# Performance work log

Measured on AMD Instinct MI355X. Metric: run time of the kernel, lower is better.

Reference implementation:

```python
import jax, jax.numpy as jnp
import numpy as np

N, E = 50000, 800000
IN_C, OUT_C, D_EMB = 64, 64, 64
NEG_SLOPE = 0.2  # GDN GraphLayer default leaky_relu slope


def setup_inputs() -> dict:
    key = jax.random.key(0)
    ks = jax.random.split(key, 9)
    return {
        "x": jax.random.normal(ks[0], (N, IN_C), jnp.float32),
        "edge_index": jax.random.randint(ks[1], (2, E), 0, N, dtype=jnp.int32),
        "embedding": jax.random.normal(ks[2], (N, D_EMB), jnp.float32),
        # learned params of GraphLayer (heads=1, concat)
        "W": jax.random.normal(ks[3], (OUT_C, IN_C), jnp.float32) * (1.0 / np.sqrt(IN_C)),
        "att_i": jax.random.normal(ks[4], (OUT_C,), jnp.float32) * 0.1,
        "att_j": jax.random.normal(ks[5], (OUT_C,), jnp.float32) * 0.1,
        "att_em_i": jax.random.normal(ks[6], (D_EMB,), jnp.float32) * 0.1,
        "att_em_j": jax.random.normal(ks[7], (D_EMB,), jnp.float32) * 0.1,
        "bias": jax.random.normal(ks[8], (OUT_C,), jnp.float32) * 0.01,
    }


def reference(x, edge_index, embedding, W, att_i, att_j, att_em_i, att_em_j, bias):
    n = x.shape[0]
    loops = jnp.arange(n, dtype=edge_index.dtype)
    src = jnp.concatenate([edge_index[0], loops])  # message source j
    dst = jnp.concatenate([edge_index[1], loops])  # message target i

    h = x @ W.T  # [N, OUT_C]
    # per-node attention scores (equivalent to cat(h, emb) . cat(att, att_em))
    s_i = h @ att_i + embedding @ att_em_i  # [N]
    s_j = h @ att_j + embedding @ att_em_j  # [N]

    alpha = s_i[dst] + s_j[src]                         # [E+N] edge logits
    alpha = jax.nn.leaky_relu(alpha, NEG_SLOPE)
    # softmax over incoming edges of each destination node
    amax = jax.ops.segment_max(alpha, dst, num_segments=n)
    ex = jnp.exp(alpha - amax[dst])
    denom = jax.ops.segment_sum(ex, dst, num_segments=n)
    alpha = ex / (denom[dst] + 1e-16)

    msg = h[src] * alpha[:, None]                       # [E+N, OUT_C]
    out = jax.ops.segment_sum(msg, dst, num_segments=n) + bias
    return jax.nn.relu(out)
```

## Files before the change

### kernel.cpp

```cpp
#include <hip/hip_runtime.h>
#include <hip/hip_bf16.h>
#include <math.h>

#define NEG_SLOPE 0.2f

#define XTA(k, r) ((k) * 64 + ((r) ^ ((((k) >> 2) & 7) << 2)))

#define NBUK 256
#define SCAT 512
#define LCAP 28
#define LSTR 29
#define FCAP 5120
#define FPAD 16

__device__ __forceinline__ void gemm_tile(
    float* lds, int t, int tid,
    const float* __restrict__ x, const float* __restrict__ emb,
    const float* __restrict__ W,
    const float* __restrict__ att_i, const float* __restrict__ att_j,
    const float* __restrict__ att_em_i, const float* __restrict__ att_em_j,
    __hip_bfloat16* __restrict__ h, float* __restrict__ s_i,
    float* __restrict__ s_j, int N)
{
    float* XT = lds;
    float* WT = lds + 4096;

    const int rbase = t * 64;
    const int valid = min(64, N - rbase);

    #pragma unroll
    for (int i = 0; i < 4; ++i) {
        int idx = i * 256 + tid;
        int r = idx >> 4, m = idx & 15;
        float4 v = make_float4(0.f, 0.f, 0.f, 0.f);
        if (r < valid)
            v = *reinterpret_cast<const float4*>(x + (size_t)(rbase + r) * 64 + 4 * m);
        int k = 4 * m;
        XT[XTA(k + 0, r)] = v.x;
        XT[XTA(k + 1, r)] = v.y;
        XT[XTA(k + 2, r)] = v.z;
        XT[XTA(k + 3, r)] = v.w;
    }
    #pragma unroll
    for (int i = 0; i < 4; ++i) {
        int idx = i * 256 + tid;
        int c = idx >> 4, m = idx & 15;
        float4 v = *reinterpret_cast<const float4*>(W + idx * 4);
        int k = 4 * m;
        WT[XTA(k + 0, c)] = v.x;
        WT[XTA(k + 1, c)] = v.y;
        WT[XTA(k + 2, c)] = v.z;
        WT[XTA(k + 3, c)] = v.w;
    }
    __syncthreads();

    const int cg_ = tid & 15, rg = tid >> 4;
    const int c0 = cg_ * 4, r0 = rg * 4;
    float acc[4][4];
    #pragma unroll
    for (int a = 0; a < 4; ++a)
        #pragma unroll
        for (int q = 0; q < 4; ++q) acc[a][q] = 0.f;

    #pragma unroll 4
    for (int k = 0; k < 64; ++k) {
        float4 wv = *reinterpret_cast<float4*>(&WT[XTA(k, c0)]);
        float4 xa = *reinterpret_cast<float4*>(&XT[XTA(k, r0)]);
        float xs[4] = {xa.x, xa.y, xa.z, xa.w};
        float ws[4] = {wv.x, wv.y, wv.z, wv.w};
        #pragma unroll
        for (int a = 0; a < 4; ++a)
            #pragma unroll
            for (int q = 0; q < 4; ++q)
                acc[a][q] = fmaf(ws[a], xs[q], acc[a][q]);
    }

    #pragma unroll
    for (int q = 0; q < 4; ++q) {
        int r = r0 + q;
        if (r < valid) {
            union { __hip_bfloat16 p[4]; uint2 u; } pk;
            pk.p[0] = __float2bfloat16(acc[0][q]);
            pk.p[1] = __float2bfloat16(acc[1][q]);
            pk.p[2] = __float2bfloat16(acc[2][q]);
            pk.p[3] = __float2bfloat16(acc[3][q]);
            *reinterpret_cast<uint2*>(h + (size_t)(rbase + r) * 64 + c0) = pk.u;
        }
    }

    float ai[4], aj[4];
    #pragma unroll
    for (int a = 0; a < 4; ++a) { ai[a] = att_i[c0 + a]; aj[a] = att_j[c0 + a]; }

    __syncthreads();
    float* RED_I = lds;
    float* RED_J = lds + 1088;
    float* EMT   = lds + 4096;

    #pragma unroll
    for (int q = 0; q < 4; ++q) {
        int r = r0 + q;
        float pi = acc[0][q]*ai[0] + acc[1][q]*ai[1] + acc[2][q]*ai[2] + acc[3][q]*ai[3];
        float pj = acc[0][q]*aj[0] + acc[1][q]*aj[1] + acc[2][q]*aj[2] + acc[3][q]*aj[3];
        RED_I[r * 17 + cg_] = pi;
        RED_J[r * 17 + cg_] = pj;
    }
    #pragma unroll
    for (int i = 0; i < 4; ++i) {
        int idx = i * 256 + tid;
        int r = idx >> 4, m = idx & 15;
        float4 v = make_float4(0.f, 0.f, 0.f, 0.f);
        if (r < valid)
            v = *reinterpret_cast<const float4*>(emb + (size_t)(rbase + r) * 64 + 4 * m);
        int k = 4 * m;
        EMT[XTA(k + 0, r)] = v.x;
        EMT[XTA(k + 1, r)] = v.y;
        EMT[XTA(k + 2, r)] = v.z;
        EMT[XTA(k + 3, r)] = v.w;
    }
    __syncthreads();

    if (tid < 64 && tid < valid) {
        float ri = 0.f, rj = 0.f;
        #pragma unroll
        for (int j = 0; j < 16; ++j) {
            ri += RED_I[tid * 17 + j];
            rj += RED_J[tid * 17 + j];
        }
        float ei = 0.f, ej = 0.f;
        #pragma unroll 16
        for (int k = 0; k < 64; ++k) {
            float ev = EMT[XTA(k, tid)];
            ei = fmaf(ev, att_em_i[k], ei);
            ej = fmaf(ev, att_em_j[k], ej);
        }
        s_i[rbase + tid] = ri + ei;
        s_j[rbase + tid] = rj + ej;
    }
}

__global__ __launch_bounds__(256) void k_gemm_scatter(
    const float* __restrict__ x, const float* __restrict__ emb,
    const float* __restrict__ W,
    const float* __restrict__ att_i, const float* __restrict__ att_j,
    const float* __restrict__ att_em_i, const float* __restrict__ att_em_j,
    const int* __restrict__ srcA, const int* __restrict__ dstA,
    int* __restrict__ fcur, unsigned* __restrict__ fifo,
    __hip_bfloat16* __restrict__ h, float* __restrict__ s_i,
    float* __restrict__ s_j, int N, int E, int sh)
{
    __shared__ float lds[8192];
    const int tid = threadIdx.x;

    if ((int)blockIdx.x < SCAT) {
        const int b2 = blockIdx.x;
        int*      lcnt  = reinterpret_cast<int*>(lds);
        unsigned* lst   = reinterpret_cast<unsigned*>(lcnt + NBUK);
        int*      lbase = reinterpret_cast<int*>(lst + NBUK * LSTR);
        for (int i = tid; i < NBUK; i += 256) lcnt[i] = 0;
        __syncthreads();

        const int npos = SCAT * 256;
        const int E4 = E >> 2;
        const int4* d4p = reinterpret_cast<const int4*>(dstA);
        const int4* s4p = reinterpret_cast<const int4*>(srcA);
        const unsigned ml = (1u << sh) - 1u;

        #define PUT(dd, ss) do {                                             \
            int _b = (int)((unsigned)(dd) >> sh);                            \
            unsigned _w = ((unsigned)(ss) << 16) | ((unsigned)(dd) & ml);    \
            int _lp = atomicAdd(&lcnt[_b], 1);                               \
            if (_lp < LCAP) lst[_b * LSTR + _lp] = _w;                       \
            else { int _gp = atomicAdd(&fcur[_b * FPAD], 1);                 \
                   if (_gp < FCAP) fifo[(size_t)_b * FCAP + _gp] = _w; }     \
        } while (0)

        for (int p = b2 * 256 + tid; p < E4; p += npos) {
            int4 d4 = d4p[p];
            int4 s4 = s4p[p];
            PUT(d4.x, s4.x);
            PUT(d4.y, s4.y);
            PUT(d4.z, s4.z);
            PUT(d4.w, s4.w);
        }
        for (int e = E4 * 4 + b2 * 256 + tid; e < E; e += npos) {
            int dd = dstA[e], ss = srcA[e];
            PUT(dd, ss);
        }
        #undef PUT
        __syncthreads();

        {
            int cnt = lcnt[tid];
            if (cnt > LCAP) cnt = LCAP;
            int base = 0;
            if (cnt > 0) base = atomicAdd(&fcur[tid * FPAD], cnt);
            lbase[tid] = base;
        }
        __syncthreads();

        const int lane = tid & 63, wid = tid >> 6;
        #pragma unroll
        for (int g = 0; g < 8; ++g) {
            int b = wid * 64 + g * 8 + (lane >> 3);
            int idx = lane & 7;
            int cnt = lcnt[b];
            if (cnt > LCAP) cnt = LCAP;
            int base = lbase[b];
            for (int i = idx; i < cnt; i += 8) {
                int gp = base + i;
                if (gp < FCAP)
                    fifo[(size_t)b * FCAP + gp] = lst[b * LSTR + i];
            }
        }
        return;
    }

    gemm_tile(lds, blockIdx.x - SCAT, tid, x, emb, W, att_i, att_j,
              att_em_i, att_em_j, h, s_i, s_j, N);
}

__global__ __launch_bounds__(1024) void k_place(
    const unsigned* __restrict__ fifo, const int* __restrict__ fcur,
    const float* __restrict__ s_i, const float* __restrict__ s_j,
    uint2* __restrict__ csr2, int* __restrict__ cursor,
    int N, int sh)
{
    __shared__ int   lcnt[256];
    __shared__ float sbuf[256];
    const int tid = threadIdx.x;
    const int b = blockIdx.x;
    const int range = 1 << sh;
    const int base = b << sh;

    for (int i = tid; i < range; i += 1024) {
        lcnt[i] = 0;
        int node = base + i;
        sbuf[i] = (node < N) ? s_i[node] : 0.f;
    }
    __syncthreads();

    int cnt = fcur[b * FPAD];
    if (cnt > FCAP) cnt = FCAP;
    const unsigned* f = fifo + (size_t)b * FCAP;
    for (int i = tid; i < cnt; i += 1024) {
        unsigned w = f[i];
        int dloc = (int)(w & (unsigned)(range - 1));
        int s = (int)(w >> 16);
        float a = sbuf[dloc] + s_j[s];
        a = (a > 0.f) ? a : NEG_SLOPE * a;
        float ex = __expf(a);
        int pos = atomicAdd(&lcnt[dloc], 1);
        if (pos < 64)
            csr2[(size_t)(base + dloc) * 64 + pos] =
                make_uint2(__float_as_uint(ex), (unsigned)s);
    }
    __syncthreads();

    for (int i = tid; i < range; i += 1024) {
        int node = base + i;
        if (node < N) cursor[node] = lcnt[i];
    }
}

__global__ __launch_bounds__(256) void k_aggregate(
    const __hip_bfloat16* __restrict__ h, const float* __restrict__ s_i,
    const float* __restrict__ s_j, const int* __restrict__ cursor,
    const uint2* __restrict__ csr2, const float* __restrict__ bias,
    float* __restrict__ out, int N)
{
    __shared__ uint2 tbl[4][64];
    const int tid  = threadIdx.x;
    const int lane = tid & 63;
    const int wid  = tid >> 6;
    const int node = (blockIdx.x * blockDim.x + tid) >> 6;
    if (node >= N) return;

    int deg_e = cursor[node];
    deg_e = (deg_e > 63) ? 63 : deg_e;

    uint2 rec = make_uint2(0u, (unsigned)node);
    if (lane < deg_e) {
        rec = csr2[(size_t)node * 64 + lane];
    } else if (lane == deg_e) {
        float a = s_i[node] + s_j[node];
        a = (a > 0.f) ? a : NEG_SLOPE * a;
        rec.x = __float_as_uint(__expf(a));
    }
    float l = __uint_as_float(rec.x);
    #pragma unroll
    for (int off = 32; off > 0; off >>= 1) l += __shfl_xor(l, off);

    tbl[wid][lane] = rec;

    const int e8 = lane >> 3;
    const int c8 = lane & 7;
    const uint4* hp4 = reinterpret_cast<const uint4*>(h);
    float a0 = 0.f, a1 = 0.f, a2 = 0.f, a3 = 0.f;
    float a4 = 0.f, a5 = 0.f, a6 = 0.f, a7 = 0.f;

    const int degT = deg_e + 1;
    const int iters = (degT + 7) >> 3;
    #pragma unroll 2
    for (int it = 0; it < iters; ++it) {
        uint2 r2 = tbl[wid][8 * it + e8];
        float e = __uint_as_float(r2.x);
        int   t = (int)r2.y;
        uint4 u = hp4[(size_t)t * 8 + c8];
        a0 = fmaf(e, __uint_as_float(u.x << 16), a0);
        a1 = fmaf(e, __uint_as_float(u.x & 0xffff0000u), a1);
        a2 = fmaf(e, __uint_as_float(u.y << 16), a2);
        a3 = fmaf(e, __uint_as_float(u.y & 0xffff0000u), a3);
        a4 = fmaf(e, __uint_as_float(u.z << 16), a4);
        a5 = fmaf(e, __uint_as_float(u.z & 0xffff0000u), a5);
        a6 = fmaf(e, __uint_as_float(u.w << 16), a6);
        a7 = fmaf(e, __uint_as_float(u.w & 0xffff0000u), a7);
    }

    a0 += __shfl_xor(a0, 8); a0 += __shfl_xor(a0, 16); a0 += __shfl_xor(a0, 32);
    a1 += __shfl_xor(a1, 8); a1 += __shfl_xor(a1, 16); a1 += __shfl_xor(a1, 32);
    a2 += __shfl_xor(a2, 8); a2 += __shfl_xor(a2, 16); a2 += __shfl_xor(a2, 32);
    a3 += __shfl_xor(a3, 8); a3 += __shfl_xor(a3, 16); a3 += __shfl_xor(a3, 32);
    a4 += __shfl_xor(a4, 8); a4 += __shfl_xor(a4, 16); a4 += __shfl_xor(a4, 32);
    a5 += __shfl_xor(a5, 8); a5 += __shfl_xor(a5, 16); a5 += __shfl_xor(a5, 32);
    a6 += __shfl_xor(a6, 8); a6 += __shfl_xor(a6, 16); a6 += __shfl_xor(a6, 32);
    a7 += __shfl_xor(a7, 8); a7 += __shfl_xor(a7, 16); a7 += __shfl_xor(a7, 32);

    if (lane < 8) {
        float inv = 1.f / (l + 1e-16f);
        float4 b0 = *reinterpret_cast<const float4*>(bias + 8 * lane);
        float4 b1 = *reinterpret_cast<const float4*>(bias + 8 * lane + 4);
        float4 o0, o1;
        o0.x = fmaxf(a0 * inv + b0.x, 0.f);
        o0.y = fmaxf(a1 * inv + b0.y, 0.f);
        o0.z = fmaxf(a2 * inv + b0.z, 0.f);
        o0.w = fmaxf(a3 * inv + b0.w, 0.f);
        o1.x = fmaxf(a4 * inv + b1.x, 0.f);
        o1.y = fmaxf(a5 * inv + b1.y, 0.f);
        o1.z = fmaxf(a6 * inv + b1.z, 0.f);
        o1.w = fmaxf(a7 * inv + b1.w, 0.f);
        *reinterpret_cast<float4*>(out + (size_t)node * 64 + 8 * lane)     = o0;
        *reinterpret_cast<float4*>(out + (size_t)node * 64 + 8 * lane + 4) = o1;
    }
}

extern "C" void kernel_launch(void* const* d_in, const int* in_sizes, int n_in,
                              void* d_out, int out_size, void* d_ws, size_t ws_size,
                              hipStream_t stream) {
    const float* x        = (const float*)d_in[0];
    const int*   ei       = (const int*)  d_in[1];
    const float* emb      = (const float*)d_in[2];
    const float* W        = (const float*)d_in[3];
    const float* att_i    = (const float*)d_in[4];
    const float* att_j    = (const float*)d_in[5];
    const float* att_em_i = (const float*)d_in[6];
    const float* att_em_j = (const float*)d_in[7];
    const float* bias     = (const float*)d_in[8];
    float* out = (float*)d_out;

    const int N = in_sizes[0] / 64;
    const int E = in_sizes[1] / 2;
    const int* e_src = ei;
    const int* e_dst = ei + E;

    char* ws = (char*)d_ws;
    __hip_bfloat16* h = (__hip_bfloat16*)ws;  ws += (size_t)N * 64 * 2;
    float* s_i     = (float*)ws;  ws += (size_t)N * 4;
    float* s_j     = (float*)ws;  ws += (size_t)N * 4;
    int*   cursor  = (int*)ws;    ws += (size_t)N * 4;
    uint2* csr2    = (uint2*)ws;  ws += (size_t)N * 64 * 8;
    unsigned* fifo = (unsigned*)ws;  ws += (size_t)NBUK * FCAP * 4;
    int*   fcur    = (int*)ws;    ws += NBUK * FPAD * 4;

    int sh = 0;
    while (((N - 1) >> sh) >= NBUK) ++sh;
    const int nbuk_eff = ((N - 1) >> sh) + 1;

    const int GB = (N + 63) / 64;

    hipMemsetAsync(fcur, 0, NBUK * FPAD * sizeof(int), stream);
    k_gemm_scatter<<<SCAT + GB, 256, 0, stream>>>(
        x, emb, W, att_i, att_j, att_em_i, att_em_j,
        e_src, e_dst, fcur, fifo, h, s_i, s_j, N, E, sh);
    k_place<<<nbuk_eff, 1024, 0, stream>>>(fifo, fcur, s_i, s_j, csr2,
                                           cursor, N, sh);
    k_aggregate<<<(N * 64 + 255) / 256, 256, 0, stream>>>(h, s_i, s_j, cursor,
                                                          csr2, bias, out, N);
}
```

Before: 145.6 us.

## Fuse place stage into gemm/scatter kernel with global completion counter

Merges the k_place kernel into the gemm/scatter kernel. Trailing blocks spin on a global atomic counter until all gemm and scatter blocks finish, which removes one kernel launch and its boundary. Gemm blocks are reordered to come first, and place blocks now run with 256 threads instead of 1024. The aggregate loop also skips gathering h rows for zero-weight edge slots. The spin-wait relies on place blocks being scheduled only after the producer blocks, which carries a deadlock risk and makes place blocks wait idle.

```diff
diff --git a/kernel.cpp b/kernel.cpp
--- a/kernel.cpp
+++ b/kernel.cpp
@@ -139,21 +139,32 @@
     }
 }
 
-__global__ __launch_bounds__(256) void k_gemm_scatter(
+__global__ __launch_bounds__(256) void k_fused(
     const float* __restrict__ x, const float* __restrict__ emb,
     const float* __restrict__ W,
     const float* __restrict__ att_i, const float* __restrict__ att_j,
     const float* __restrict__ att_em_i, const float* __restrict__ att_em_j,
     const int* __restrict__ srcA, const int* __restrict__ dstA,
     int* __restrict__ fcur, unsigned* __restrict__ fifo,
+    int* __restrict__ done,
     __hip_bfloat16* __restrict__ h, float* __restrict__ s_i,
-    float* __restrict__ s_j, int N, int E, int sh)
+    float* __restrict__ s_j, uint2* __restrict__ csr2,
+    int* __restrict__ cursor, int N, int E, int GB, int sh)
 {
     __shared__ float lds[8192];
     const int tid = threadIdx.x;
-
-    if ((int)blockIdx.x < SCAT) {
-        const int b2 = blockIdx.x;
+    const int bx  = (int)blockIdx.x;
+
+    if (bx < GB) {
+        gemm_tile(lds, bx, tid, x, emb, W, att_i, att_j,
+                  att_em_i, att_em_j, h, s_i, s_j, N);
+        __syncthreads();
+        if (tid == 0) { __threadfence(); atomicAdd(done, 1); }
+        return;
+    }
+
+    if (bx < GB + SCAT) {
+        const int b2 = bx - GB;
         int*      lcnt  = reinterpret_cast<int*>(lds);
         unsigned* lst   = reinterpret_cast<unsigned*>(lcnt + NBUK);
         int*      lbase = reinterpret_cast<int*>(lst + NBUK * LSTR);
@@ -213,53 +224,53 @@
                     fifo[(size_t)b * FCAP + gp] = lst[b * LSTR + i];
             }
         }
+        __syncthreads();
+        if (tid == 0) { __threadfence(); atomicAdd(done, 1); }
         return;
     }
 
-    gemm_tile(lds, blockIdx.x - SCAT, tid, x, emb, W, att_i, att_j,
-              att_em_i, att_em_j, h, s_i, s_j, N);
-}
-
-__global__ __launch_bounds__(1024) void k_place(
-    const unsigned* __restrict__ fifo, const int* __restrict__ fcur,
-    const float* __restrict__ s_i, const float* __restrict__ s_j,
-    uint2* __restrict__ csr2, int* __restrict__ cursor,
-    int N, int sh)
-{
-    __shared__ int   lcnt[256];
-    __shared__ float sbuf[256];
-    const int tid = threadIdx.x;
-    const int b = blockIdx.x;
-    const int range = 1 << sh;
-    const int base = b << sh;
-
-    for (int i = tid; i < range; i += 1024) {
-        lcnt[i] = 0;
-        int node = base + i;
-        sbuf[i] = (node < N) ? s_i[node] : 0.f;
-    }
-    __syncthreads();
-
-    int cnt = fcur[b * FPAD];
-    if (cnt > FCAP) cnt = FCAP;
-    const unsigned* f = fifo + (size_t)b * FCAP;
-    for (int i = tid; i < cnt; i += 1024) {
-        unsigned w = f[i];
-        int dloc = (int)(w & (unsigned)(range - 1));
-        int s = (int)(w >> 16);
-        float a = sbuf[dloc] + s_j[s];
-        a = (a > 0.f) ? a : NEG_SLOPE * a;
-        float ex = __expf(a);
-        int pos = atomicAdd(&lcnt[dloc], 1);
-        if (pos < 64)
-            csr2[(size_t)(base + dloc) * 64 + pos] =
-                make_uint2(__float_as_uint(ex), (unsigned)s);
-    }
-    __syncthreads();
-
-    for (int i = tid; i < range; i += 1024) {
-        int node = base + i;
-        if (node < N) cursor[node] = lcnt[i];
+    {
+        const int b = bx - GB - SCAT;
+        int*   lcnt2 = reinterpret_cast<int*>(lds);
+        float* sbuf  = lds + 256;
+        const int range = 1 << sh;
+        const int base = b << sh;
+
+        if (tid == 0) {
+            while (atomicAdd(done, 0) < GB + SCAT)
+                __builtin_amdgcn_s_sleep(8);
+        }
+        __syncthreads();
+        __threadfence();
+
+        for (int i = tid; i < range; i += 256) {
+            lcnt2[i] = 0;
+            int node = base + i;
+            sbuf[i] = (node < N) ? s_i[node] : 0.f;
+        }
+        __syncthreads();
+
+        int cnt = fcur[b * FPAD];
+        if (cnt > FCAP) cnt = FCAP;
+        const unsigned* f = fifo + (size_t)b * FCAP;
+        for (int i = tid; i < cnt; i += 256) {
+            unsigned w = f[i];
+            int dloc = (int)(w & (unsigned)(range - 1));
+            int s = (int)(w >> 16);
+            float a = sbuf[dloc] + s_j[s];
+            a = (a > 0.f) ? a : NEG_SLOPE * a;
+            float ex = __expf(a);
+            int pos = atomicAdd(&lcnt2[dloc], 1);
+            if (pos < 64)
+                csr2[(size_t)(base + dloc) * 64 + pos] =
+                    make_uint2(__float_as_uint(ex), (unsigned)s);
+        }
+        __syncthreads();
+
+        for (int i = tid; i < range; i += 256) {
+            int node = base + i;
+            if (node < N) cursor[node] = lcnt2[i];
+        }
     }
 }
 
@@ -305,16 +316,18 @@
     for (int it = 0; it < iters; ++it) {
         uint2 r2 = tbl[wid][8 * it + e8];
         float e = __uint_as_float(r2.x);
-        int   t = (int)r2.y;
-        uint4 u = hp4[(size_t)t * 8 + c8];
-        a0 = fmaf(e, __uint_as_float(u.x << 16), a0);
-        a1 = fmaf(e, __uint_as_float(u.x & 0xffff0000u), a1);
-        a2 = fmaf(e, __uint_as_float(u.y << 16), a2);
-        a3 = fmaf(e, __uint_as_float(u.y & 0xffff0000u), a3);
-        a4 = fmaf(e, __uint_as_float(u.z << 16), a4);
-        a5 = fmaf(e, __uint_as_float(u.z & 0xffff0000u), a5);
-        a6 = fmaf(e, __uint_as_float(u.w << 16), a6);
-        a7 = fmaf(e, __uint_as_float(u.w & 0xffff0000u), a7);
+        if (e != 0.f) {
+            int   t = (int)r2.y;
+            uint4 u = hp4[(size_t)t * 8 + c8];
+            a0 = fmaf(e, __uint_as_float(u.x << 16), a0);
+            a1 = fmaf(e, __uint_as_float(u.x & 0xffff0000u), a1);
+            a2 = fmaf(e, __uint_as_float(u.y << 16), a2);
+            a3 = fmaf(e, __uint_as_float(u.y & 0xffff0000u), a3);
+            a4 = fmaf(e, __uint_as_float(u.z << 16), a4);
+            a5 = fmaf(e, __uint_as_float(u.z & 0xffff0000u), a5);
+            a6 = fmaf(e, __uint_as_float(u.w << 16), a6);
+            a7 = fmaf(e, __uint_as_float(u.w & 0xffff0000u), a7);
+        }
     }
 
     a0 += __shfl_xor(a0, 8); a0 += __shfl_xor(a0, 16); a0 += __shfl_xor(a0, 32);
@@ -371,6 +384,7 @@
     uint2* csr2    = (uint2*)ws;  ws += (size_t)N * 64 * 8;
     unsigned* fifo = (unsigned*)ws;  ws += (size_t)NBUK * FCAP * 4;
     int*   fcur    = (int*)ws;    ws += NBUK * FPAD * 4;
+    int*   done    = (int*)ws;    ws += 64;
 
     int sh = 0;
     while (((N - 1) >> sh) >= NBUK) ++sh;
@@ -378,12 +392,11 @@
 
     const int GB = (N + 63) / 64;
 
-    hipMemsetAsync(fcur, 0, NBUK * FPAD * sizeof(int), stream);
-    k_gemm_scatter<<<SCAT + GB, 256, 0, stream>>>(
+    hipMemsetAsync(fcur, 0, (size_t)NBUK * FPAD * 4 + 64, stream);
+    k_fused<<<GB + SCAT + nbuk_eff, 256, 0, stream>>>(
         x, emb, W, att_i, att_j, att_em_i, att_em_j,
-        e_src, e_dst, fcur, fifo, h, s_i, s_j, N, E, sh);
-    k_place<<<nbuk_eff, 1024, 0, stream>>>(fifo, fcur, s_i, s_j, csr2,
-                                           cursor, N, sh);
+        e_src, e_dst, fcur, fifo, done, h, s_i, s_j, csr2, cursor,
+        N, E, GB, sh);
     k_aggregate<<<(N * 64 + 255) / 256, 256, 0, stream>>>(h, s_i, s_j, cursor,
                                                           csr2, bias, out, N);
 }
```

Measured after the change: 250.1 us. 71.8% more time.
